# Kernel optimization log

Measured on AMD Instinct MI355X. Metric: run time of the kernel, lower is better.

## Reference

```python
import jax, jax.numpy as jnp
import numpy as np
import math

B, S, D, H = 2, 2048, 1024, 16
HD = D // H  # head_dim = 64
ROPE_BASE = 100000
EPS = 1e-09


def _linear_init(key, in_f, out_f):
    std = min(1.0, math.sqrt(out_f / in_f)) / math.sqrt(in_f)
    return jax.random.normal(key, (in_f, out_f)) * std


def setup_inputs() -> dict:
    key = jax.random.key(0)
    ks = jax.random.split(key, 7)
    Q = jax.random.normal(ks[0], (B, S, D), dtype=jnp.float32)
    K = jax.random.normal(ks[1], (B, S, D), dtype=jnp.float32)
    V = jax.random.normal(ks[2], (B, S, D), dtype=jnp.float32)
    mask = jnp.tril(jnp.ones((S, S), dtype=bool))  # causal
    Wq = _linear_init(ks[3], D, D)
    Wk = _linear_init(ks[4], D, D)
    Wv = _linear_init(ks[5], D, D)
    Wo = _linear_init(ks[6], D, D)
    return {"Q": Q, "K": K, "V": V, "mask": mask,
            "Wq": Wq, "Wk": Wk, "Wv": Wv, "Wo": Wo}


def _rope_tables(seq_len, d):
    positions = jnp.arange(0, seq_len)
    freqs = ROPE_BASE ** (jnp.arange(0, d, 2) / d)
    gamma = positions[:, None] * (1.0 / freqs)[None, :]  # [t, d/2]
    return jnp.cos(gamma).astype(jnp.bfloat16), jnp.sin(gamma).astype(jnp.bfloat16)


def _apply_rope(x, cos, sin):
    # x: [..., t, d]; cos/sin: [t, d/2]
    d = x.shape[-1]
    x1, x2 = x[..., : d // 2], x[..., d // 2:]
    y1 = x1 * cos + x2 * sin
    y2 = -x1 * sin + x2 * cos
    return jnp.concatenate([y1, y2], axis=-1)


def _rms_norm(x):
    rms = jnp.sqrt(jnp.mean(jnp.square(x), axis=-1, keepdims=True) + EPS)
    return x / rms


def reference(Q, K, V, mask, Wq, Wk, Wv, Wo):
    cos, sin = _rope_tables(S, HD)
    q = jnp.dot(Q, Wq)
    k = jnp.dot(K, Wk)
    v = jnp.dot(V, Wv)
    # [B, S, D] -> [B, H, S, HD]
    split = lambda t: t.reshape(*t.shape[:-1], H, HD).swapaxes(-3, -2)
    q, k, v = split(q), split(k), split(v)
    q = _rms_norm(_apply_rope(q, cos, sin))
    k = _rms_norm(_apply_rope(k, cos, sin))
    logits = jnp.einsum('bhqd,bhkd->bhqk', q, k) / jnp.sqrt(jnp.float32(HD))
    logits = jnp.where(mask[None, None, :, :], logits, -1000000000.0)
    attn = jax.nn.softmax(logits, axis=-1)
    vals = jnp.einsum('bhqk,bhkd->bhqd', attn, v)
    # [B, H, S, HD] -> [B, S, D]
    vals = vals.swapaxes(-3, -2).reshape(B, S, D)
    return jnp.dot(vals, Wo)
```

## Files before the change

kernel.cpp:

```cpp
#include <hip/hip_runtime.h>
#include <hip/hip_bf16.h>
#include <stdint.h>

typedef __hip_bfloat16 bf16;
typedef __attribute__((ext_vector_type(8))) short short8;
typedef __attribute__((ext_vector_type(4))) short short4v;
typedef __attribute__((ext_vector_type(4))) float float4v;

static constexpr int nB = 2, nS = 2048, nD = 1024, nH = 16, nHD = 64;
static constexpr int nBS = nB * nS;

#define AS_GLOBAL __attribute__((address_space(1)))
#define AS_LDS    __attribute__((address_space(3)))

union Frag16B { short8 v; uint4 u4; uint2 u2[2]; };

__device__ __forceinline__ void gload_lds16(const void* g, void* l) {
  __builtin_amdgcn_global_load_lds((AS_GLOBAL uint32_t*)(g), (AS_LDS uint32_t*)(l), 16, 0, 0);
}

__device__ __forceinline__ float fast_exp2(float x) {
#if __has_builtin(__builtin_amdgcn_exp2f)
  return __builtin_amdgcn_exp2f(x);
#else
  float r; asm volatile("v_exp_f32 %0, %1" : "=v"(r) : "v"(x)); return r;
#endif
}

__device__ __forceinline__ void lds_barrier() {
  asm volatile("s_waitcnt lgkmcnt(0)\ns_barrier" ::: "memory");
}

__device__ __forceinline__ void lgkm_wait() {
  asm volatile("s_waitcnt lgkmcnt(0)" ::: "memory");
}

__global__ __launch_bounds__(256) void prep_kernel(
    const float* __restrict__ Qin, const float* __restrict__ Kin, const float* __restrict__ Vin,
    const float* __restrict__ Wq, const float* __restrict__ Wk,
    const float* __restrict__ Wv, const float* __restrict__ Wo,
    bf16* __restrict__ Qbf, bf16* __restrict__ Kbf, bf16* __restrict__ Vbf,
    bf16* __restrict__ WqT, bf16* __restrict__ WkT, bf16* __restrict__ WvT, bf16* __restrict__ WoT,
    bf16* __restrict__ cos_t, bf16* __restrict__ sin_t) {
  __shared__ float tile[64][65];
  int bx = blockIdx.x, t = threadIdx.x;
  if (bx < 3072) {
    int tz = bx >> 10, blk = bx & 1023;
    const float* src = tz == 0 ? Qin : tz == 1 ? Kin : Vin;
    bf16* dst = tz == 0 ? Qbf : tz == 1 ? Kbf : Vbf;
#pragma unroll
    for (int i = 0; i < 4; ++i) {
      int idx = blk * 1024 + i * 256 + t;
      float4 v = ((const float4*)src)[idx];
      union { bf16 b[4]; uint2 u; } tmp;
      tmp.b[0] = __float2bfloat16(v.x);
      tmp.b[1] = __float2bfloat16(v.y);
      tmp.b[2] = __float2bfloat16(v.z);
      tmp.b[3] = __float2bfloat16(v.w);
      ((uint2*)dst)[idx] = tmp.u;
    }
  } else if (bx < 4096) {
    int idx = bx - 3072;
    int z = idx >> 8;
    const float* W = z == 0 ? Wq : z == 1 ? Wk : z == 2 ? Wv : Wo;
    bf16* T = z == 0 ? WqT : z == 1 ? WkT : z == 2 ? WvT : WoT;
    int tk = (idx & 15) * 64, tn = ((idx >> 4) & 15) * 64;
    int c = t & 63, r0 = t >> 6;
#pragma unroll
    for (int i = 0; i < 16; ++i) {
      int r = i * 4 + r0;
      tile[r][c] = W[(size_t)(tk + r) * nD + tn + c];
    }
    __syncthreads();
#pragma unroll
    for (int i = 0; i < 16; ++i) {
      int r = i * 4 + r0;
      T[(size_t)(tn + r) * nD + tk + c] = __float2bfloat16(tile[c][r]);
    }
  } else {
    int base = (bx - 4096) * 1024 + t * 4;
#pragma unroll
    for (int i = 0; i < 4; ++i) {
      int e = base + i;
      int s = e >> 5, j = e & 31;
      float inv_freq = powf(100000.0f, -(float)(2 * j) / 64.0f);
      float g = (float)s * inv_freq;
      cos_t[e] = __float2bfloat16(cosf(g));
      sin_t[e] = __float2bfloat16(sinf(g));
    }
  }
}

__global__ __launch_bounds__(256, 2) void gemm_qkv_kernel(
    const bf16* __restrict__ A0, const bf16* __restrict__ A1, const bf16* __restrict__ A2,
    const bf16* __restrict__ Bt0, const bf16* __restrict__ Bt1, const bf16* __restrict__ Bt2,
    bf16* __restrict__ q_h, bf16* __restrict__ k_h, bf16* __restrict__ vt_h,
    const bf16* __restrict__ cos_t, const bf16* __restrict__ sin_t) {
  const int bid = blockIdx.x;
  const int swz = (bid & 7) * 96 + (bid >> 3);
  const int z = swz >> 8;
  const int rem = swz & 255;
  const int n0 = (rem >> 5) * 128;
  const int m0 = (rem & 31) * 128;

  const bf16* __restrict__ A  = z == 0 ? A0 : (z == 1 ? A1 : A2);
  const bf16* __restrict__ Bt = z == 0 ? Bt0 : (z == 1 ? Bt1 : Bt2);

  __shared__ bf16 As[2 * 128 * 64];
  __shared__ bf16 Bs[2 * 128 * 64];

  const int t = threadIdx.x;
  const int lane = t & 63;
  const int wid = t >> 6;
  const int quad = lane >> 4;
  const int l16 = lane & 15;
  const int r7 = l16 & 7;
  const int wm = wid >> 1;
  const int wn = wid & 1;

  const int srow = t >> 3;
  const int scg8 = ((t & 7) ^ (srow & 7)) * 8;

  const int ch0 = (quad ^ r7) * 8;
  const int ch1 = ch0 ^ 32;
  const int arow = (wm * 64 + l16) * 64;
  const int brow = (wn * 64 + l16) * 64;

#define STAGE(KT, BUF) do { \
    const bf16* ag_ = A + (size_t)(m0 + srow) * nD + (KT) * 64 + scg8; \
    const bf16* bg_ = Bt + (size_t)(n0 + srow) * nD + (KT) * 64 + scg8; \
    _Pragma("unroll") \
    for (int i = 0; i < 4; ++i) { \
      gload_lds16(ag_ + (size_t)(i * 32) * nD, As + (BUF) + i * 2048 + wid * 512); \
      gload_lds16(bg_ + (size_t)(i * 32) * nD, Bs + (BUF) + i * 2048 + wid * 512); \
    } \
  } while (0)

  float4v acc[4][4] = {};

  STAGE(0, 0);
  asm volatile("s_waitcnt vmcnt(0)" ::: "memory");
  __builtin_amdgcn_s_barrier();

#pragma unroll 2
  for (int T = 0; T < 16; ++T) {
    const int cu = (T & 1) * 8192;
    const int nx = cu ^ 8192;

    if (T < 15) STAGE(T + 1, nx);

    Frag16B fa0[4], fa1[4], fb0[4], fb1[4];
#pragma unroll
    for (int mi = 0; mi < 4; ++mi) {
      fa0[mi].u4 = *(const uint4*)&As[cu + arow + mi * 1024 + ch0];
      fa1[mi].u4 = *(const uint4*)&As[cu + arow + mi * 1024 + ch1];
    }
#pragma unroll
    for (int ni = 0; ni < 4; ++ni) {
      fb0[ni].u4 = *(const uint4*)&Bs[cu + brow + ni * 1024 + ch0];
      fb1[ni].u4 = *(const uint4*)&Bs[cu + brow + ni * 1024 + ch1];
    }

    __builtin_amdgcn_s_setprio(1);
#pragma unroll
    for (int mi = 0; mi < 4; ++mi)
#pragma unroll
      for (int ni = 0; ni < 4; ++ni)
        acc[mi][ni] = __builtin_amdgcn_mfma_f32_16x16x32_bf16(fa0[mi].v, fb0[ni].v, acc[mi][ni], 0, 0, 0);
#pragma unroll
    for (int mi = 0; mi < 4; ++mi)
#pragma unroll
      for (int ni = 0; ni < 4; ++ni)
        acc[mi][ni] = __builtin_amdgcn_mfma_f32_16x16x32_bf16(fa1[mi].v, fb1[ni].v, acc[mi][ni], 0, 0, 0);
    __builtin_amdgcn_s_setprio(0);

    asm volatile("s_waitcnt vmcnt(0)" ::: "memory");
    __builtin_amdgcn_s_barrier();
  }
#undef STAGE

  const int col0 = n0 + wn * 64;
  if (z <= 1) {
    bf16* dst = z ? k_h : q_h;
#pragma unroll
    for (int mi = 0; mi < 4; ++mi)
#pragma unroll
      for (int r = 0; r < 4; ++r) {
        int row = m0 + wm * 64 + mi * 16 + quad * 4 + r;
        int s = row & (nS - 1);
        float x0 = acc[mi][0][r], x1 = acc[mi][1][r], x2 = acc[mi][2][r], x3 = acc[mi][3][r];
        float y[4];
#pragma unroll
        for (int p = 0; p < 2; ++p) {
          int d = p * 16 + l16;
          float c = __bfloat162float(cos_t[s * 32 + d]);
          float sn = __bfloat162float(sin_t[s * 32 + d]);
          float xa = p ? x1 : x0, xb = p ? x3 : x2;
          y[p] = xa * c + xb * sn;
          y[p + 2] = xb * c - xa * sn;
        }
        float ss = y[0] * y[0] + y[1] * y[1] + y[2] * y[2] + y[3] * y[3];
#pragma unroll
        for (int m = 1; m <= 8; m <<= 1) ss += __shfl_xor(ss, m, 64);
        float inv = 1.0f / sqrtf(ss * (1.0f / 64.0f) + 1e-9f);
#pragma unroll
        for (int ni = 0; ni < 4; ++ni)
          dst[(size_t)row * nD + col0 + ni * 16 + l16] = __float2bfloat16(y[ni] * inv);
      }
  } else {
#pragma unroll
    for (int mi = 0; mi < 4; ++mi)
#pragma unroll
      for (int r = 0; r < 4; ++r) {
        int row = m0 + wm * 64 + mi * 16 + quad * 4 + r;
        int b = row >> 11, s = row & (nS - 1);
#pragma unroll
        for (int ni = 0; ni < 4; ++ni) {
          int col = col0 + ni * 16 + l16;
          int h = col >> 6, d = col & 63;
          vt_h[((size_t)((b * nH + h) * 64 + d)) * nS + s] = __float2bfloat16(acc[mi][ni][r]);
        }
      }
  }
}

__global__ __launch_bounds__(256, 2) void gemm_out_kernel(
    const bf16* __restrict__ A, const bf16* __restrict__ Bt, float* __restrict__ C) {
  __shared__ bf16 As[2 * 64 * 64];
  __shared__ bf16 Bs[2 * 128 * 64];
  const int bid = blockIdx.x;
  const int n0 = (bid & 7) * 128;
  const int m0 = (bid >> 3) * 64;
  const int t = threadIdx.x;
  const int lane = t & 63;
  const int wid = t >> 6;
  const int quad = lane >> 4;
  const int l16 = lane & 15;
  const int r7 = l16 & 7;
  const int wm = wid >> 1;
  const int wn = wid & 1;

  const int srow = t >> 3;
  const int scg8 = ((t & 7) ^ (srow & 7)) * 8;

  const int ch0 = (quad ^ r7) * 8;
  const int ch1 = ch0 ^ 32;
  const int arow = (wm * 32 + l16) * 64;
  const int brow = (wn * 64 + l16) * 64;

#define STAGE_O(KT, AB, BB) do { \
    const bf16* ag_ = A + (size_t)(m0 + srow) * nD + (KT) * 64 + scg8; \
    const bf16* bg_ = Bt + (size_t)(n0 + srow) * nD + (KT) * 64 + scg8; \
    gload_lds16(ag_, As + (AB) + wid * 512); \
    gload_lds16(ag_ + (size_t)32 * nD, As + (AB) + 2048 + wid * 512); \
    _Pragma("unroll") \
    for (int i = 0; i < 4; ++i) \
      gload_lds16(bg_ + (size_t)(i * 32) * nD, Bs + (BB) + i * 2048 + wid * 512); \
  } while (0)

  float4v acc[2][4] = {};

  STAGE_O(0, 0, 0);
  asm volatile("s_waitcnt vmcnt(0)" ::: "memory");
  __builtin_amdgcn_s_barrier();

#pragma unroll 2
  for (int T = 0; T < 16; ++T) {
    const int cua = (T & 1) * 4096;
    const int cub = (T & 1) * 8192;

    if (T < 15) STAGE_O(T + 1, cua ^ 4096, cub ^ 8192);

    Frag16B a0[2], a1[2], b0[4], b1[4];
#pragma unroll
    for (int mi = 0; mi < 2; ++mi) {
      a0[mi].u4 = *(const uint4*)&As[cua + arow + mi * 1024 + ch0];
      a1[mi].u4 = *(const uint4*)&As[cua + arow + mi * 1024 + ch1];
    }
#pragma unroll
    for (int ni = 0; ni < 4; ++ni) {
      b0[ni].u4 = *(const uint4*)&Bs[cub + brow + ni * 1024 + ch0];
      b1[ni].u4 = *(const uint4*)&Bs[cub + brow + ni * 1024 + ch1];
    }

    __builtin_amdgcn_s_setprio(1);
#pragma unroll
    for (int mi = 0; mi < 2; ++mi)
#pragma unroll
      for (int ni = 0; ni < 4; ++ni)
        acc[mi][ni] = __builtin_amdgcn_mfma_f32_16x16x32_bf16(a0[mi].v, b0[ni].v, acc[mi][ni], 0, 0, 0);
#pragma unroll
    for (int mi = 0; mi < 2; ++mi)
#pragma unroll
      for (int ni = 0; ni < 4; ++ni)
        acc[mi][ni] = __builtin_amdgcn_mfma_f32_16x16x32_bf16(a1[mi].v, b1[ni].v, acc[mi][ni], 0, 0, 0);
    __builtin_amdgcn_s_setprio(0);

    asm volatile("s_waitcnt vmcnt(0)" ::: "memory");
    __builtin_amdgcn_s_barrier();
  }
#undef STAGE_O

#pragma unroll
  for (int mi = 0; mi < 2; ++mi)
#pragma unroll
    for (int ni = 0; ni < 4; ++ni)
#pragma unroll
      for (int r = 0; r < 4; ++r) {
        int row = m0 + wm * 32 + mi * 16 + quad * 4 + r;
        int col = n0 + wn * 64 + ni * 16 + l16;
        C[(size_t)row * nD + col] = acc[mi][ni][r];
      }
}

static constexpr float SC = 0.18033688011112042f;

__global__ __launch_bounds__(512, 4) void attn_kernel(const bf16* __restrict__ q_h,
                                                      const bf16* __restrict__ k_h,
                                                      const bf16* __restrict__ vt_h,
                                                      bf16* __restrict__ vals) {
  __shared__ bf16 lds_buf[4 * 8192];

  const int t = threadIdx.x;
  const int lane = t & 63, wid = t >> 6, quad = lane >> 4, l16 = lane & 15;
  const int id = blockIdx.x;
  const int xcd = id & 7;
  const int j = id >> 3;
  const int jj = j & 31;
  const int bh = xcd * 4 + (jj & 3);
  const int u = jj >> 2;
  const int qt = (j < 32) ? (15 - u) : u;
  const int b = bh >> 4, h = bh & 15;

  const bf16* Kbase = k_h + ((size_t)b * nS) * nD + h * 64;
  const bf16* Vbase = vt_h + (size_t)bh * 64 * nS;

  const int rl = lane >> 3;
  const int cg8 = ((lane & 7) ^ rl) * 8;
  const int r7 = l16 & 7;

  bf16* const scratch = lds_buf + wid * 1152;

  const int q0w = qt * 128 + wid * 16;

  Frag16B qf[2];
  {
    const bf16* qp = q_h + ((size_t)(b * nS + q0w + l16)) * nD + h * 64;
    qf[0].u4 = *(const uint4*)(qp + quad * 8);
    qf[1].u4 = *(const uint4*)(qp + 32 + quad * 8);
  }

#define STAGE_KV(KT) do { \
    const int bo_ = ((KT) & 1) * 8192; \
    const bf16* kg_ = Kbase + (size_t)((KT) * 128 + wid * 16 + rl) * nD + cg8; \
    gload_lds16(kg_, lds_buf + bo_ + wid * 1024); \
    gload_lds16(kg_ + (size_t)8 * nD, lds_buf + bo_ + wid * 1024 + 512); \
    const bf16* vg_ = Vbase + (size_t)(wid * 8 + rl) * nS + (KT) * 128 + cg8; \
    gload_lds16(vg_, lds_buf + 16384 + bo_ + wid * 512); \
    gload_lds16(vg_ + 64, lds_buf + 16384 + bo_ + 4096 + wid * 512); \
  } while (0)

#define QKH(Kb, HB, ST) do { \
    _Pragma("unroll") \
    for (int kt4 = 0; kt4 < 4; ++kt4) { \
      int row = (HB) * 64 + kt4 * 16 + l16; \
      Frag16B k0_, k1_; \
      k0_.u4 = *(const uint4*)&(Kb)[row * 64 + ((quad ^ r7) * 8)]; \
      k1_.u4 = *(const uint4*)&(Kb)[row * 64 + (((quad + 4) ^ r7) * 8)]; \
      float4v zz_ = {}; \
      zz_ = __builtin_amdgcn_mfma_f32_16x16x32_bf16(k0_.v, qf[0].v, zz_, 0, 0, 0); \
      (ST)[kt4] = __builtin_amdgcn_mfma_f32_16x16x32_bf16(k1_.v, qf[1].v, zz_, 0, 0, 0); \
    } \
  } while (0)

#define EXPH(ST, PF) do { \
    _Pragma("unroll") \
    for (int kt4 = 0; kt4 < 4; ++kt4) \
      _Pragma("unroll") \
      for (int r = 0; r < 4; ++r) { \
        float p_ = fast_exp2((ST)[kt4][r] * SC); \
        l_acc += p_; \
        union { bf16 hh; short ss; } cv_; \
        cv_.hh = __float2bfloat16(p_); \
        (PF)[kt4][r] = cv_.ss; \
      } \
  } while (0)

#define EXPHM(ST, PF, HB) do { \
    int qg_ = q0w + l16; \
    _Pragma("unroll") \
    for (int kt4 = 0; kt4 < 4; ++kt4) { \
      int key0_ = qt * 128 + (HB) * 64 + kt4 * 16 + quad * 4; \
      _Pragma("unroll") \
      for (int r = 0; r < 4; ++r) { \
        float x_ = (ST)[kt4][r] * SC; \
        if (key0_ + r > qg_) x_ = -12000.0f; \
        float p_ = fast_exp2(x_); \
        l_acc += p_; \
        union { bf16 hh; short ss; } cv_; \
        cv_.hh = __float2bfloat16(p_); \
        (PF)[kt4][r] = cv_.ss; \
      } \
    } \
  } while (0)

#define PVH(Vb, HB, PF) do { \
    _Pragma("unroll") \
    for (int dt = 0; dt < 4; ++dt) { \
      int row = dt * 16 + l16; \
      _Pragma("unroll") \
      for (int kt4 = 0; kt4 < 4; ++kt4) { \
        int chunk_ = kt4 * 2 + (quad >> 1); \
        union { uint2 u; short4v s; } vv_; \
        vv_.u = *(const uint2*)&(Vb)[(HB) * 4096 + row * 64 + ((chunk_ ^ r7) * 8) + (quad & 1) * 4]; \
        o_acc[dt] = __builtin_amdgcn_mfma_f32_16x16x16bf16_1k(vv_.s, (PF)[kt4], o_acc[dt], 0, 0, 0); \
      } \
    } \
  } while (0)

  STAGE_KV(0);
  asm volatile("s_waitcnt vmcnt(0)" ::: "memory");
  __builtin_amdgcn_s_barrier();

  float4v o_acc[4] = {};
  float l_acc = 0.f;

  for (int kt = 0; kt < qt; ++kt) {
    STAGE_KV(kt + 1);
    const bf16* Kb = lds_buf + (kt & 1) * 8192;
    const bf16* Vb = lds_buf + 16384 + (kt & 1) * 8192;

    float4v st0[4], st1[4];
    __builtin_amdgcn_s_setprio(1);
    QKH(Kb, 0, st0);
    QKH(Kb, 1, st1);
    __builtin_amdgcn_s_setprio(0);

    short4v pf[4];
    EXPH(st0, pf);
    __builtin_amdgcn_s_setprio(1);
    PVH(Vb, 0, pf);
    __builtin_amdgcn_s_setprio(0);
    EXPH(st1, pf);
    __builtin_amdgcn_s_setprio(1);
    PVH(Vb, 1, pf);
    __builtin_amdgcn_s_setprio(0);

    asm volatile("s_waitcnt vmcnt(0) lgkmcnt(0)" ::: "memory");
    __builtin_amdgcn_s_barrier();
  }

  {
    const bf16* Kb = lds_buf + (qt & 1) * 8192;
    const bf16* Vb = lds_buf + 16384 + (qt & 1) * 8192;

    float4v st0[4];
    QKH(Kb, 0, st0);
    short4v pf[4];
    EXPHM(st0, pf, 0);
    PVH(Vb, 0, pf);

    if (wid >= 4) {
      float4v st1[4];
      QKH(Kb, 1, st1);
      EXPHM(st1, pf, 1);
      PVH(Vb, 1, pf);
    }
  }
#undef STAGE_KV
#undef QKH
#undef EXPH
#undef EXPHM
#undef PVH

  lds_barrier();

  float la = l_acc;
  la += __shfl_xor(la, 16, 64);
  la += __shfl_xor(la, 32, 64);
  float inv_l = 1.0f / la;
#pragma unroll
  for (int dt = 0; dt < 4; ++dt) {
    union { bf16 b2[2]; uint u; } p01, p23;
    p01.b2[0] = __float2bfloat16(o_acc[dt][0] * inv_l);
    p01.b2[1] = __float2bfloat16(o_acc[dt][1] * inv_l);
    p23.b2[0] = __float2bfloat16(o_acc[dt][2] * inv_l);
    p23.b2[1] = __float2bfloat16(o_acc[dt][3] * inv_l);
    *(uint*)&scratch[l16 * 72 + dt * 16 + quad * 4] = p01.u;
    *(uint*)&scratch[l16 * 72 + dt * 16 + quad * 4 + 2] = p23.u;
  }
  lgkm_wait();
  uint4 r0 = *(const uint4*)&scratch[l16 * 72 + quad * 16];
  uint4 r1 = *(const uint4*)&scratch[l16 * 72 + quad * 16 + 8];
  int qrow = q0w + l16;
  bf16* vp = vals + ((size_t)(b * nS + qrow)) * nD + h * 64 + quad * 16;
  *(uint4*)(vp) = r0;
  *(uint4*)(vp + 8) = r1;
}

extern "C" void kernel_launch(void* const* d_in, const int* in_sizes, int n_in,
                              void* d_out, int out_size, void* d_ws, size_t ws_size,
                              hipStream_t stream) {
  const float* Qin = (const float*)d_in[0];
  const float* Kin = (const float*)d_in[1];
  const float* Vin = (const float*)d_in[2];
  const float* Wq = (const float*)d_in[4];
  const float* Wk = (const float*)d_in[5];
  const float* Wv = (const float*)d_in[6];
  const float* Wo = (const float*)d_in[7];
  float* out = (float*)d_out;

  char* ws = (char*)d_ws;
  const size_t MB = 1u << 20;
  bf16* Qbf = (bf16*)(ws + 0 * MB);
  bf16* Kbf = (bf16*)(ws + 8 * MB);
  bf16* Vbf = (bf16*)(ws + 16 * MB);
  bf16* WqT = (bf16*)(ws + 24 * MB);
  bf16* WkT = (bf16*)(ws + 26 * MB);
  bf16* WvT = (bf16*)(ws + 28 * MB);
  bf16* WoT = (bf16*)(ws + 30 * MB);
  bf16* cos_t = (bf16*)(ws + 32 * MB);
  bf16* sin_t = (bf16*)(ws + 33 * MB);
  bf16* q_h = (bf16*)(ws + 34 * MB);
  bf16* k_h = (bf16*)(ws + 42 * MB);
  bf16* vt_h = (bf16*)(ws + 50 * MB);
  bf16* vals = (bf16*)(ws + 58 * MB);

  prep_kernel<<<4160, 256, 0, stream>>>(Qin, Kin, Vin, Wq, Wk, Wv, Wo,
                                        Qbf, Kbf, Vbf, WqT, WkT, WvT, WoT, cos_t, sin_t);

  gemm_qkv_kernel<<<768, 256, 0, stream>>>(Qbf, Kbf, Vbf, WqT, WkT, WvT,
                                           q_h, k_h, vt_h, cos_t, sin_t);

  attn_kernel<<<512, 512, 0, stream>>>(q_h, k_h, vt_h, vals);

  gemm_out_kernel<<<512, 256, 0, stream>>>(vals, WoT, out);
}
```

Measured before the change: 216.6 us.

## Halve QKV GEMM k-tile to 32 to fit three blocks per CU

```diff
diff --git a/kernel.cpp b/kernel.cpp
--- a/kernel.cpp
+++ b/kernel.cpp
@@ -91,7 +91,7 @@
   }
 }
 
-__global__ __launch_bounds__(256, 2) void gemm_qkv_kernel(
+__global__ __launch_bounds__(256, 3) void gemm_qkv_kernel(
     const bf16* __restrict__ A0, const bf16* __restrict__ A1, const bf16* __restrict__ A2,
     const bf16* __restrict__ Bt0, const bf16* __restrict__ Bt1, const bf16* __restrict__ Bt2,
     bf16* __restrict__ q_h, bf16* __restrict__ k_h, bf16* __restrict__ vt_h,
@@ -106,78 +106,72 @@
   const bf16* __restrict__ A  = z == 0 ? A0 : (z == 1 ? A1 : A2);
   const bf16* __restrict__ Bt = z == 0 ? Bt0 : (z == 1 ? Bt1 : Bt2);
 
-  __shared__ bf16 As[2 * 128 * 64];
-  __shared__ bf16 Bs[2 * 128 * 64];
+  __shared__ bf16 As[2 * 128 * 32];
+  __shared__ bf16 Bs[2 * 128 * 32];
 
   const int t = threadIdx.x;
   const int lane = t & 63;
   const int wid = t >> 6;
   const int quad = lane >> 4;
   const int l16 = lane & 15;
-  const int r7 = l16 & 7;
   const int wm = wid >> 1;
   const int wn = wid & 1;
 
-  const int srow = t >> 3;
-  const int scg8 = ((t & 7) ^ (srow & 7)) * 8;
-
-  const int ch0 = (quad ^ r7) * 8;
-  const int ch1 = ch0 ^ 32;
-  const int arow = (wm * 64 + l16) * 64;
-  const int brow = (wn * 64 + l16) * 64;
-
-#define STAGE(KT, BUF) do { \
-    const bf16* ag_ = A + (size_t)(m0 + srow) * nD + (KT) * 64 + scg8; \
-    const bf16* bg_ = Bt + (size_t)(n0 + srow) * nD + (KT) * 64 + scg8; \
-    _Pragma("unroll") \
-    for (int i = 0; i < 4; ++i) { \
-      gload_lds16(ag_ + (size_t)(i * 32) * nD, As + (BUF) + i * 2048 + wid * 512); \
-      gload_lds16(bg_ + (size_t)(i * 32) * nD, Bs + (BUF) + i * 2048 + wid * 512); \
-    } \
+  const int sc    = (t & 7) ^ ((t >> 3) & 7);
+  const int sml   = 2 * (t >> 3) + (sc >> 2);
+  const int skoff = (sc & 3) * 8;
+  const int swave = wid * 512;
+
+  const int R0a = wm * 32 + (l16 >> 1);
+  const int R0b = wn * 32 + (l16 >> 1);
+  const int cpar = (l16 & 1) * 4;
+  const int abase = R0a * 64 + (((cpar + quad) ^ (R0a & 7)) * 8);
+  const int bbase = R0b * 64 + (((cpar + quad) ^ (R0b & 7)) * 8);
+
+#define STAGE_A(KT, BUF) do { \
+    const bf16* ag_ = A + (size_t)(m0 + sml) * nD + (KT) * 32 + skoff; \
+    gload_lds16(ag_, As + (BUF) + swave); \
+    gload_lds16(ag_ + (size_t)64 * nD, As + (BUF) + 2048 + swave); \
+  } while (0)
+#define STAGE_B(KT, BUF) do { \
+    const bf16* bg_ = Bt + (size_t)(n0 + sml) * nD + (KT) * 32 + skoff; \
+    gload_lds16(bg_, Bs + (BUF) + swave); \
+    gload_lds16(bg_ + (size_t)64 * nD, Bs + (BUF) + 2048 + swave); \
   } while (0)
 
   float4v acc[4][4] = {};
 
-  STAGE(0, 0);
+  STAGE_A(0, 0);
+  STAGE_B(0, 0);
   asm volatile("s_waitcnt vmcnt(0)" ::: "memory");
   __builtin_amdgcn_s_barrier();
 
 #pragma unroll 2
-  for (int T = 0; T < 16; ++T) {
-    const int cu = (T & 1) * 8192;
-    const int nx = cu ^ 8192;
-
-    if (T < 15) STAGE(T + 1, nx);
-
-    Frag16B fa0[4], fa1[4], fb0[4], fb1[4];
-#pragma unroll
-    for (int mi = 0; mi < 4; ++mi) {
-      fa0[mi].u4 = *(const uint4*)&As[cu + arow + mi * 1024 + ch0];
-      fa1[mi].u4 = *(const uint4*)&As[cu + arow + mi * 1024 + ch1];
-    }
-#pragma unroll
-    for (int ni = 0; ni < 4; ++ni) {
-      fb0[ni].u4 = *(const uint4*)&Bs[cu + brow + ni * 1024 + ch0];
-      fb1[ni].u4 = *(const uint4*)&Bs[cu + brow + ni * 1024 + ch1];
-    }
+  for (int T = 0; T < 32; ++T) {
+    const int cu = (T & 1) * 4096;
+    const int nx = cu ^ 4096;
+
+    if (T < 31) { STAGE_A(T + 1, nx); STAGE_B(T + 1, nx); }
+
+    Frag16B fa[4], fb[4];
+#pragma unroll
+    for (int mi = 0; mi < 4; ++mi) fa[mi].u4 = *(const uint4*)&As[cu + abase + mi * 512];
+#pragma unroll
+    for (int ni = 0; ni < 4; ++ni) fb[ni].u4 = *(const uint4*)&Bs[cu + bbase + ni * 512];
 
     __builtin_amdgcn_s_setprio(1);
 #pragma unroll
     for (int mi = 0; mi < 4; ++mi)
 #pragma unroll
       for (int ni = 0; ni < 4; ++ni)
-        acc[mi][ni] = __builtin_amdgcn_mfma_f32_16x16x32_bf16(fa0[mi].v, fb0[ni].v, acc[mi][ni], 0, 0, 0);
-#pragma unroll
-    for (int mi = 0; mi < 4; ++mi)
-#pragma unroll
-      for (int ni = 0; ni < 4; ++ni)
-        acc[mi][ni] = __builtin_amdgcn_mfma_f32_16x16x32_bf16(fa1[mi].v, fb1[ni].v, acc[mi][ni], 0, 0, 0);
+        acc[mi][ni] = __builtin_amdgcn_mfma_f32_16x16x32_bf16(fa[mi].v, fb[ni].v, acc[mi][ni], 0, 0, 0);
     __builtin_amdgcn_s_setprio(0);
 
     asm volatile("s_waitcnt vmcnt(0)" ::: "memory");
     __builtin_amdgcn_s_barrier();
   }
-#undef STAGE
+#undef STAGE_A
+#undef STAGE_B
 
   const int col0 = n0 + wn * 64;
   if (z <= 1) {
```

Measured after the change: 214.5 us. No clear change (-0.9%).

## Single-buffer QKV GEMM LDS tiles to raise occupancy to three blocks per CU

Applied to the files above, without the earlier changes.

```diff
diff --git a/kernel.cpp b/kernel.cpp
--- a/kernel.cpp
+++ b/kernel.cpp
@@ -91,7 +91,7 @@
   }
 }
 
-__global__ __launch_bounds__(256, 2) void gemm_qkv_kernel(
+__global__ __launch_bounds__(256, 3) void gemm_qkv_kernel(
     const bf16* __restrict__ A0, const bf16* __restrict__ A1, const bf16* __restrict__ A2,
     const bf16* __restrict__ Bt0, const bf16* __restrict__ Bt1, const bf16* __restrict__ Bt2,
     bf16* __restrict__ q_h, bf16* __restrict__ k_h, bf16* __restrict__ vt_h,
@@ -106,8 +106,8 @@
   const bf16* __restrict__ A  = z == 0 ? A0 : (z == 1 ? A1 : A2);
   const bf16* __restrict__ Bt = z == 0 ? Bt0 : (z == 1 ? Bt1 : Bt2);
 
-  __shared__ bf16 As[2 * 128 * 64];
-  __shared__ bf16 Bs[2 * 128 * 64];
+  __shared__ bf16 As[128 * 64];
+  __shared__ bf16 Bs[128 * 64];
 
   const int t = threadIdx.x;
   const int lane = t & 63;
@@ -126,39 +126,31 @@
   const int arow = (wm * 64 + l16) * 64;
   const int brow = (wn * 64 + l16) * 64;
 
-#define STAGE(KT, BUF) do { \
-    const bf16* ag_ = A + (size_t)(m0 + srow) * nD + (KT) * 64 + scg8; \
-    const bf16* bg_ = Bt + (size_t)(n0 + srow) * nD + (KT) * 64 + scg8; \
-    _Pragma("unroll") \
-    for (int i = 0; i < 4; ++i) { \
-      gload_lds16(ag_ + (size_t)(i * 32) * nD, As + (BUF) + i * 2048 + wid * 512); \
-      gload_lds16(bg_ + (size_t)(i * 32) * nD, Bs + (BUF) + i * 2048 + wid * 512); \
-    } \
-  } while (0)
-
   float4v acc[4][4] = {};
 
-  STAGE(0, 0);
-  asm volatile("s_waitcnt vmcnt(0)" ::: "memory");
-  __builtin_amdgcn_s_barrier();
-
-#pragma unroll 2
   for (int T = 0; T < 16; ++T) {
-    const int cu = (T & 1) * 8192;
-    const int nx = cu ^ 8192;
-
-    if (T < 15) STAGE(T + 1, nx);
+    {
+      const bf16* ag_ = A + (size_t)(m0 + srow) * nD + T * 64 + scg8;
+      const bf16* bg_ = Bt + (size_t)(n0 + srow) * nD + T * 64 + scg8;
+#pragma unroll
+      for (int i = 0; i < 4; ++i) {
+        gload_lds16(ag_ + (size_t)(i * 32) * nD, As + i * 2048 + wid * 512);
+        gload_lds16(bg_ + (size_t)(i * 32) * nD, Bs + i * 2048 + wid * 512);
+      }
+    }
+    asm volatile("s_waitcnt vmcnt(0)" ::: "memory");
+    __builtin_amdgcn_s_barrier();
 
     Frag16B fa0[4], fa1[4], fb0[4], fb1[4];
 #pragma unroll
     for (int mi = 0; mi < 4; ++mi) {
-      fa0[mi].u4 = *(const uint4*)&As[cu + arow + mi * 1024 + ch0];
-      fa1[mi].u4 = *(const uint4*)&As[cu + arow + mi * 1024 + ch1];
+      fa0[mi].u4 = *(const uint4*)&As[arow + mi * 1024 + ch0];
+      fa1[mi].u4 = *(const uint4*)&As[arow + mi * 1024 + ch1];
     }
 #pragma unroll
     for (int ni = 0; ni < 4; ++ni) {
-      fb0[ni].u4 = *(const uint4*)&Bs[cu + brow + ni * 1024 + ch0];
-      fb1[ni].u4 = *(const uint4*)&Bs[cu + brow + ni * 1024 + ch1];
+      fb0[ni].u4 = *(const uint4*)&Bs[brow + ni * 1024 + ch0];
+      fb1[ni].u4 = *(const uint4*)&Bs[brow + ni * 1024 + ch1];
     }
 
     __builtin_amdgcn_s_setprio(1);
@@ -174,10 +166,8 @@
         acc[mi][ni] = __builtin_amdgcn_mfma_f32_16x16x32_bf16(fa1[mi].v, fb1[ni].v, acc[mi][ni], 0, 0, 0);
     __builtin_amdgcn_s_setprio(0);
 
-    asm volatile("s_waitcnt vmcnt(0)" ::: "memory");
     __builtin_amdgcn_s_barrier();
   }
-#undef STAGE
 
   const int col0 = n0 + wn * 64;
   if (z <= 1) {
```

Measured after the change: 210.2 us. 1.03x faster.
